# Optimization experiments

Measured on AMD Instinct MI355X. Metric: run time of the kernel, lower is better.

Reference implementation:

```python
import jax, jax.numpy as jnp
import numpy as np

EPS = 1e-5
EMBED_DIM = 1024
CTX_DIM = 768
NUM_HEADS = 16
DH = EMBED_DIM // NUM_HEADS
# Faithful to torch source: embed_dim // num_heads ** 0.5 parses as embed_dim // (num_heads**0.5)
SCALE = EMBED_DIM // (NUM_HEADS ** 0.5)  # = 256.0


def ws_conv1x1(x, w, b, mask):
    # weight-standardized 1x1 conv1d: w [O, I, 1], x [B, I, T]
    w2 = w[..., 0]
    mu = jnp.mean(w2, axis=1, keepdims=True)
    var = jnp.var(w2, axis=1, keepdims=True)
    wn = (w2 - mu) * jax.lax.rsqrt(var + EPS)
    y = jnp.einsum('oi,bit->bot', wn, x) + b[None, :, None]
    if mask is not None:
        y = jnp.where(mask, y, 0.0)  # mask [B,1,T] bool
    return y


def layernorm(x, g, b):
    # normalize over last axis
    mu = jnp.mean(x, axis=-1, keepdims=True)
    var = jnp.var(x, axis=-1, keepdims=True)
    return (x - mu) * jax.lax.rsqrt(var + EPS) * g + b


def setup_inputs() -> dict:
    key = jax.random.key(0)
    ks = jax.random.split(key, 16)
    B, T, S = 4, 1024, 1024
    inp = {
        'x': jax.random.normal(ks[0], (B, EMBED_DIM, T), dtype=jnp.float32),
        'context': jax.random.normal(ks[1], (B, CTX_DIM, S), dtype=jnp.float32),
        'mask': jax.random.randint(ks[2], (B, 1, T), 0, 2).astype(bool),
        'mask_ctx': jax.random.randint(ks[3], (B, 1, S), 0, 2).astype(bool),
        'qw': jax.random.normal(ks[4], (EMBED_DIM, EMBED_DIM, 1), dtype=jnp.float32) * 0.02,
        'qb': jnp.zeros((EMBED_DIM,), jnp.float32),
        'kw': jax.random.normal(ks[5], (EMBED_DIM, CTX_DIM, 1), dtype=jnp.float32) * 0.02,
        'kb': jnp.zeros((EMBED_DIM,), jnp.float32),
        'vw': jax.random.normal(ks[6], (EMBED_DIM, CTX_DIM, 1), dtype=jnp.float32) * 0.02,
        'vb': jnp.zeros((EMBED_DIM,), jnp.float32),
        'ow': jax.random.normal(ks[7], (EMBED_DIM, EMBED_DIM, 1), dtype=jnp.float32) * 0.02,
        'ob': jnp.zeros((EMBED_DIM,), jnp.float32),
        'gq': jnp.ones((DH,), jnp.float32), 'bq': jnp.zeros((DH,), jnp.float32),
        'gk': jnp.ones((DH,), jnp.float32), 'bk': jnp.zeros((DH,), jnp.float32),
        'gv': jnp.ones((DH,), jnp.float32), 'bv': jnp.zeros((DH,), jnp.float32),
    }
    return inp


def reference(x, context, mask, mask_ctx, qw, qb, kw, kb, vw, vb, ow, ob, gq, bq, gk, bk, gv, bv):
    B, E, T = x.shape
    S = context.shape[-1]
    q = ws_conv1x1(x, qw, qb, mask)            # [B,E,T]
    k = ws_conv1x1(context, kw, kb, mask_ctx)  # [B,E,S]
    v = ws_conv1x1(context, vw, vb, mask_ctx)  # [B,E,S]
    # split heads -> [B,H,dh,L]
    q = q.reshape(B, NUM_HEADS, DH, T)
    k = k.reshape(B, NUM_HEADS, DH, S)
    v = v.reshape(B, NUM_HEADS, DH, S)
    # middle_norm: LayerNorm over dh (applied on transposed layout)
    q = jnp.swapaxes(layernorm(jnp.swapaxes(q, -1, -2), gq, bq), -1, -2)
    k = jnp.swapaxes(layernorm(jnp.swapaxes(k, -1, -2), gk, bk), -1, -2)
    v = jnp.swapaxes(layernorm(jnp.swapaxes(v, -1, -2), gv, bv), -1, -2)
    # scores: k^T @ q -> [B,H,S,T]
    scores = jnp.einsum('bhds,bhdt->bhst', k, q) / SCALE
    scores = jnp.where(mask[:, :, None, :], scores, -1e9)  # mask over query dim T
    scores = jax.nn.softmax(scores, axis=-1)               # softmax over T (as in source)
    scores = jnp.where(mask_ctx[:, :, :, None], scores, 0.0)
    out = jnp.einsum('bhds,bhst->bhdt', v, scores)          # v @ scores -> [B,H,dh,T]
    out = out.reshape(B, E, T)
    out = ws_conv1x1(out, ow, ob, mask) + x
    return out
```

## Files before the change

kernel.cpp:

```cpp
#include <hip/hip_runtime.h>

#define NB 4
#define TT 1024
#define SS 1024
#define EE 1024
#define CCH 768
#define NH 16
#define DHH 64
#define EPSF 1e-5f
#define QSCALE (1.4426950408889634f / 256.0f)

typedef unsigned short u16;
typedef __attribute__((ext_vector_type(8))) short short8;
typedef __attribute__((ext_vector_type(8))) unsigned short u16x8;
typedef __attribute__((ext_vector_type(4))) unsigned short u16x4;
typedef __attribute__((ext_vector_type(4))) float f32x4;

__device__ __forceinline__ u16 f2bu(float f) {
    union { float f; unsigned u; } x; x.f = f;
    unsigned r = x.u + 0x7fffu + ((x.u >> 16) & 1u);
    return (u16)(r >> 16);
}
__device__ __forceinline__ float bu2f(u16 u) {
    union { unsigned u; float f; } x; x.u = ((unsigned)u) << 16; return x.f;
}

#if __has_builtin(__builtin_amdgcn_exp2f)
#define EXP2(x) __builtin_amdgcn_exp2f(x)
#else
#define EXP2(x) exp2f(x)
#endif

#define MFMA16(a, b, c) __builtin_amdgcn_mfma_f32_16x16x32_bf16((a), (b), (c), 0, 0, 0)

__device__ __forceinline__ void gload16(const void* g, void* l) {
    __builtin_amdgcn_global_load_lds(
        (const __attribute__((address_space(1))) void*)g,
        (__attribute__((address_space(3))) void*)l, 16, 0, 0);
}

template<int R>
__device__ __forceinline__ void stage_tile(
    const u16* __restrict__ g, int ldg, u16* lds, int w, int lane) {
    constexpr int PW = R / 32;
    int r0 = lane >> 3;
    int cs = ((lane & 7) << 4) ^ (r0 << 4);
#pragma unroll
    for (int j = 0; j < PW; j++) {
        int inst = w * PW + j;
        const u16* src = g + (size_t)(inst * 8 + r0) * ldg + (cs >> 1);
        gload16(src, lds + inst * 512);
    }
}

__device__ __forceinline__ const u16* swz_ptr(const u16* tile, int row, int col) {
    int off = row * 128 + ((col * 2) ^ ((row & 7) << 4));
    return (const u16*)((const char*)tile + off);
}

#define PREP_WS_END   4096
#define PREP_SCAN_END (PREP_WS_END + 8)
#define PREP_TR_END   (PREP_SCAN_END + 1792)
#define PREP_FILL_END (PREP_TR_END + 4096)

__global__ __launch_bounds__(256) void prep(
    const float* __restrict__ qw, const float* __restrict__ kw,
    const float* __restrict__ vw, const float* __restrict__ ow,
    u16* __restrict__ wqn, u16* __restrict__ wkn,
    u16* __restrict__ wvn, u16* __restrict__ won,
    const float* __restrict__ x, const float* __restrict__ ctx,
    const int* __restrict__ mask, const int* __restrict__ mask_ctx,
    u16* __restrict__ xc, u16* __restrict__ cc,
    int* __restrict__ tIdx, int* __restrict__ sIdx,
    int* __restrict__ cntQ, int* __restrict__ cntK,
    float* __restrict__ outF) {
    __shared__ float tile[64][65];
    __shared__ int spos[64], smask[64], wtoti[4];
    __shared__ float sa[4], sb2[4], smean, srstd;
    int bid = blockIdx.x, tid = threadIdx.x;

    if (bid < PREP_WS_END) {
        int mat = bid >> 10, row = bid & 1023;
        const float* w = mat == 0 ? qw : (mat == 1 ? kw : (mat == 2 ? vw : ow));
        u16* wn = mat == 0 ? wqn : (mat == 1 ? wkn : (mat == 2 ? wvn : won));
        int I = (mat == 1 || mat == 2) ? CCH : EE;
        const float* wr = w + (size_t)row * I;
        float s = 0.f, s2 = 0.f;
        for (int i = tid; i < I; i += 256) { float v = wr[i]; s += v; s2 += v * v; }
#pragma unroll
        for (int off = 32; off > 0; off >>= 1) { s += __shfl_down(s, off); s2 += __shfl_down(s2, off); }
        int wid = tid >> 6;
        if ((tid & 63) == 0) { sa[wid] = s; sb2[wid] = s2; }
        __syncthreads();
        if (tid == 0) {
            float ts = sa[0] + sa[1] + sa[2] + sa[3];
            float ts2 = sb2[0] + sb2[1] + sb2[2] + sb2[3];
            float mean = ts / (float)I;
            float var = ts2 / (float)I - mean * mean;
            smean = mean; srstd = rsqrtf(var + EPSF);
        }
        __syncthreads();
        float mean = smean, r = srstd;
        u16* wo = wn + (size_t)row * I;
        for (int i = tid; i < I; i += 256) wo[i] = f2bu((wr[i] - mean) * r);
        return;
    }
    if (bid < PREP_SCAN_END) {
        int t = bid - PREP_WS_END;
        int which = t & 1, b = t >> 1;
        const int* m = (which ? mask_ctx : mask) + b * 1024;
        int* idx = (which ? sIdx : tIdx) + b * 1024;
        int* cnt = (which ? cntK : cntQ) + b;
        int base = tid * 4;
        int v[4]; int s = 0;
#pragma unroll
        for (int i = 0; i < 4; i++) { v[i] = m[base + i] ? 1 : 0; s += v[i]; }
        int lane = tid & 63, wid = tid >> 6;
        int inc = s;
#pragma unroll
        for (int off = 1; off < 64; off <<= 1) {
            int o = __shfl_up(inc, off);
            if (lane >= off) inc += o;
        }
        if (lane == 63) wtoti[wid] = inc;
        __syncthreads();
        int woff = 0;
        for (int i = 0; i < wid; i++) woff += wtoti[i];
        int p = woff + inc - s;
#pragma unroll
        for (int i = 0; i < 4; i++) {
            if (v[i]) idx[p] = base + i;
            p += v[i];
        }
        if (tid == 255) *cnt = p;
        return;
    }
    if (bid < PREP_TR_END) {
        int t = bid - PREP_SCAN_END;
        int xb = t & 15; int rem = t >> 4;
        int yy = rem % 28, b = rem / 28;
        int mat = yy < 16 ? 0 : 1;
        int r0 = (mat == 0 ? yy : yy - 16) * 64;
        int R = mat == 0 ? EE : CCH;
        const float* in = mat == 0 ? x : ctx;
        const int* m = (mat == 0 ? mask : mask_ctx) + (size_t)b * 1024;
        u16* out = mat == 0 ? xc : cc;
        int c0 = xb * 64;
        const float* ip = in + (size_t)b * R * 1024;
        u16* op = out + (size_t)b * R * 1024;
#pragma unroll
        for (int mm = 0; mm < 16; mm++) {
            int id = tid + 256 * mm; int r = id >> 6, c = id & 63;
            tile[r][c] = ip[(size_t)(r0 + r) * 1024 + c0 + c];
        }
        int base = tid * 4;
        int v[4]; int s = 0;
#pragma unroll
        for (int i = 0; i < 4; i++) { v[i] = m[base + i] ? 1 : 0; s += v[i]; }
        int lane = tid & 63, wid = tid >> 6;
        int inc = s;
#pragma unroll
        for (int off = 1; off < 64; off <<= 1) {
            int o = __shfl_up(inc, off);
            if (lane >= off) inc += o;
        }
        if (lane == 63) wtoti[wid] = inc;
        __syncthreads();
        int woff = 0;
        for (int i = 0; i < wid; i++) woff += wtoti[i];
        int p = woff + inc - s;
#pragma unroll
        for (int i = 0; i < 4; i++) {
            int g = base + i;
            if (g >= c0 && g < c0 + 64) { spos[g - c0] = p; smask[g - c0] = v[i]; }
            p += v[i];
        }
        __syncthreads();
#pragma unroll
        for (int mm = 0; mm < 16; mm++) {
            int id = tid + 256 * mm; int rr = id >> 6, cc2 = id & 63;
            if (smask[rr])
                op[(size_t)spos[rr] * R + r0 + cc2] = f2bu(tile[cc2][rr]);
        }
        return;
    }
    {
        int f = bid - PREP_TR_END;
        int b = f >> 10, o = f & 1023;
        const float* xr = x + ((size_t)b * EE + o) * TT;
        float* orow = outF + ((size_t)b * EE + o) * TT;
        const int* mrow = mask + (size_t)b * TT;
        int4 mv = ((const int4*)mrow)[tid];
        float4 xv = ((const float4*)xr)[tid];
        int t4 = tid * 4;
        if (!mv.x) orow[t4 + 0] = xv.x;
        if (!mv.y) orow[t4 + 1] = xv.y;
        if (!mv.z) orow[t4 + 2] = xv.z;
        if (!mv.w) orow[t4 + 3] = xv.w;
    }
}

__device__ __forceinline__ void gemm_core(
    const u16* __restrict__ A, const u16* __restrict__ Bp, int I,
    int o0, int l0, u16 (*at)[128][64], u16 (*bt)[64][64], f32x4 (&acc)[4][2]) {
    int tid = threadIdx.x;
    int w = tid >> 6, lane = tid & 63, quad = lane >> 4, l16 = lane & 15;
    int wm = w & 1, wn = w >> 1;
    const u16* Ab = A + (size_t)o0 * I;
    const u16* Bb = Bp + (size_t)l0 * I;
    stage_tile<128>(Ab, I, &at[0][0][0], w, lane);
    stage_tile<64>(Bb, I, &bt[0][0][0], w, lane);
    __syncthreads();
    int cur = 0;
    for (int k0 = 0; k0 < I; k0 += 64, cur ^= 1) {
        int kn = k0 + 64;
        if (kn < I) {
            stage_tile<128>(Ab + kn, I, &at[cur ^ 1][0][0], w, lane);
            stage_tile<64>(Bb + kn, I, &bt[cur ^ 1][0][0], w, lane);
        }
#pragma unroll
        for (int ks = 0; ks < 64; ks += 32) {
            short8 af[4], bf[2];
#pragma unroll
            for (int i = 0; i < 4; i++)
                af[i] = *(const short8*)swz_ptr(&at[cur][0][0], wm * 64 + i * 16 + l16, ks + quad * 8);
#pragma unroll
            for (int j = 0; j < 2; j++)
                bf[j] = *(const short8*)swz_ptr(&bt[cur][0][0], wn * 32 + j * 16 + l16, ks + quad * 8);
#pragma unroll
            for (int mt = 0; mt < 4; mt++)
#pragma unroll
                for (int nt = 0; nt < 2; nt++)
                    acc[mt][nt] = MFMA16(af[mt], bf[nt], acc[mt][nt]);
        }
        __syncthreads();
    }
}

__global__ __launch_bounds__(256) void proj_qkv(
    const u16* __restrict__ wq, const u16* __restrict__ wk, const u16* __restrict__ wv,
    const u16* __restrict__ xc, const u16* __restrict__ cc,
    const float* __restrict__ qb, const float* __restrict__ kb, const float* __restrict__ vbi,
    const int* __restrict__ cntQ, const int* __restrict__ cntK,
    const float* __restrict__ gq, const float* __restrict__ bq,
    const float* __restrict__ gk, const float* __restrict__ bk,
    const float* __restrict__ gv, const float* __restrict__ bv,
    u16* __restrict__ qc, u16* __restrict__ kc, u16* __restrict__ vn) {
    int mat = blockIdx.x >> 3;
    int o0 = (blockIdx.x & 7) * 128;
    int l0 = blockIdx.y * 64;
    int b = blockIdx.z;
    int limit = (mat == 0) ? cntQ[b] : cntK[b];
    if (l0 >= limit) return;
    __shared__ u16 at[2][128][64];
    __shared__ u16 bt[2][64][64];
    __shared__ float sg[64], sbe[64], sbias[128];
    int tid = threadIdx.x;
    int w = tid >> 6, lane = tid & 63, quad = lane >> 4, l16 = lane & 15;
    int wm = w & 1, wn = w >> 1;
    const u16* A = mat == 0 ? wq : (mat == 1 ? wk : wv);
    const u16* BT = mat == 0 ? xc : cc;
    const float* bias = mat == 0 ? qb : (mat == 1 ? kb : vbi);
    int I = mat == 0 ? EE : CCH;
    if (tid < 64) {
        const float* gsrc = mat == 0 ? gq : (mat == 1 ? gk : gv);
        const float* bsrc = mat == 0 ? bq : (mat == 1 ? bk : bv);
        sg[tid] = gsrc[tid];
        sbe[tid] = bsrc[tid];
    }
    if (tid < 128) sbias[tid] = bias[o0 + tid];

    f32x4 acc[4][2] = {};
    gemm_core(A, BT + (size_t)b * 1024 * I, I, o0, l0, at, bt, acc);

    float scale = mat == 0 ? QSCALE : 1.0f;
    int h = (o0 >> 6) + wm;
    int bh = b * NH + h;
#pragma unroll
    for (int nt = 0; nt < 2; nt++) {
        int l = l0 + wn * 32 + nt * 16 + l16;
        float vbuf[16];
        float s = 0.f;
#pragma unroll
        for (int mt = 0; mt < 4; mt++)
#pragma unroll
            for (int reg = 0; reg < 4; reg++) {
                float v = acc[mt][nt][reg] + sbias[wm * 64 + mt * 16 + quad * 4 + reg];
                vbuf[mt * 4 + reg] = v; s += v;
            }
        s += __shfl_xor(s, 16); s += __shfl_xor(s, 32);
        float mean = s * (1.f / 64);
        float s2 = 0.f;
#pragma unroll
        for (int i = 0; i < 16; i++) { float dv = vbuf[i] - mean; s2 += dv * dv; }
        s2 += __shfl_xor(s2, 16); s2 += __shfl_xor(s2, 32);
        float r = rsqrtf(s2 * (1.f / 64) + EPSF);
        if (l < limit) {
            if (mat < 2) {
                u16* outT = mat == 0 ? qc : kc;
                u16* op = outT + ((size_t)bh * 1024 + l) * 64;
#pragma unroll
                for (int mt = 0; mt < 4; mt++) {
                    u16x4 pk;
#pragma unroll
                    for (int reg = 0; reg < 4; reg++) {
                        int d = mt * 16 + quad * 4 + reg;
                        pk[reg] = f2bu(((vbuf[mt * 4 + reg] - mean) * r * sg[d] + sbe[d]) * scale);
                    }
                    *(u16x4*)&op[mt * 16 + quad * 4] = pk;
                }
            } else {
#pragma unroll
                for (int mt = 0; mt < 4; mt++)
#pragma unroll
                    for (int reg = 0; reg < 4; reg++) {
                        int d = mt * 16 + quad * 4 + reg;
                        vn[((size_t)b * EE + h * 64 + d) * 1024 + l] =
                            f2bu((vbuf[mt * 4 + reg] - mean) * r * sg[d] + sbe[d]);
                    }
            }
        }
    }
}

__global__ __launch_bounds__(256) void attn_stats_mfma(
    const u16* __restrict__ qc, const u16* __restrict__ kc,
    const int* __restrict__ cntQ, const int* __restrict__ cntK,
    float* __restrict__ lneg) {
    int s0 = blockIdx.x * 64, h = blockIdx.y, b = blockIdx.z;
    int Sc = cntK[b], Tc = cntQ[b];
    if (s0 >= Sc) return;
    __shared__ u16 kt[64][64];
    __shared__ u16 qt[2][64][64];
    __shared__ float lp[4][64];
    int tid = threadIdx.x;
    int w = tid >> 6, lane = tid & 63, quad = lane >> 4, l16 = lane & 15;
    int head = b * NH + h;
    const u16* kp = kc + (size_t)head * SS * DHH;
    const u16* qp = qc + (size_t)head * TT * DHH;
    stage_tile<64>(kp + (size_t)s0 * DHH, DHH, &kt[0][0], w, lane);
    stage_tile<64>(qp, DHH, &qt[0][0][0], w, lane);
    __syncthreads();
    float rl[4][4] = {};
    int cur = 0;
    for (int t0 = 0; t0 < Tc; t0 += 64, cur ^= 1) {
        if (t0 + 64 < Tc)
            stage_tile<64>(qp + (size_t)(t0 + 64) * DHH, DHH, &qt[cur ^ 1][0][0], w, lane);
        f32x4 acc[4] = {};
#pragma unroll
        for (int ks = 0; ks < 64; ks += 32) {
            short8 bf = *(const short8*)swz_ptr(&qt[cur][0][0], w * 16 + l16, ks + quad * 8);
#pragma unroll
            for (int mt = 0; mt < 4; mt++) {
                short8 af = *(const short8*)swz_ptr(&kt[0][0], mt * 16 + l16, ks + quad * 8);
                acc[mt] = MFMA16(af, bf, acc[mt]);
            }
        }
        int tcol = t0 + w * 16 + l16;
        if (tcol < Tc) {
#pragma unroll
            for (int mt = 0; mt < 4; mt++)
#pragma unroll
                for (int reg = 0; reg < 4; reg++)
                    rl[mt][reg] += EXP2(acc[mt][reg]);
        }
        __syncthreads();
    }
#pragma unroll
    for (int mt = 0; mt < 4; mt++) {
#pragma unroll
        for (int reg = 0; reg < 4; reg++) {
            float v = rl[mt][reg];
            v += __shfl_xor(v, 1); v += __shfl_xor(v, 2);
            v += __shfl_xor(v, 4); v += __shfl_xor(v, 8);
            if (l16 == 0) lp[w][mt * 16 + quad * 4 + reg] = v;
        }
    }
    __syncthreads();
    if (tid < 64 && s0 + tid < Sc) {
        float lv = lp[0][tid] + lp[1][tid] + lp[2][tid] + lp[3][tid];
        lneg[(size_t)head * SS + s0 + tid] = -log2f(fmaxf(lv, 1e-30f));
    }
}

__global__ __launch_bounds__(256) void attn_pv_mfma(
    const u16* __restrict__ qc, const u16* __restrict__ kc, const u16* __restrict__ vn,
    const int* __restrict__ cntQ, const int* __restrict__ cntK,
    const float* __restrict__ lneg, u16* __restrict__ ac) {
    int t0 = blockIdx.x * 64, h = blockIdx.y, b = blockIdx.z;
    int Tc = cntQ[b], Sc = cntK[b];
    if (t0 >= Tc) return;
    __shared__ u16 qt[64][64];
    __shared__ u16 kt[2][64][64];
    __shared__ u16 vt[2][64][64];
    __shared__ u16 pt[64][72];
    __shared__ float sln[SS];
    int tid = threadIdx.x;
    int w = tid >> 6, lane = tid & 63, quad = lane >> 4, l16 = lane & 15;
    int head = b * NH + h;
    const u16* qp = qc + (size_t)head * TT * DHH;
    const u16* kp = kc + (size_t)head * SS * DHH;
    const u16* vp = vn + ((size_t)head * DHH) * SS;
    for (int i = tid; i < SS; i += 256) sln[i] = lneg[(size_t)head * SS + i];
    stage_tile<64>(qp + (size_t)t0 * DHH, DHH, &qt[0][0], w, lane);
    stage_tile<64>(kp, DHH, &kt[0][0][0], w, lane);
    stage_tile<64>(vp, SS, &vt[0][0][0], w, lane);
    __syncthreads();
    int tl = w * 16 + l16;
    f32x4 oacc[4] = {};
    int cur = 0;
    for (int s0 = 0; s0 < Sc; s0 += 64, cur ^= 1) {
        int sn = s0 + 64;
        if (sn < Sc) {
            stage_tile<64>(kp + (size_t)sn * DHH, DHH, &kt[cur ^ 1][0][0], w, lane);
            stage_tile<64>(vp + sn, SS, &vt[cur ^ 1][0][0], w, lane);
        }
        f32x4 acc[4] = {};
#pragma unroll
        for (int ks = 0; ks < 64; ks += 32) {
            short8 bf = *(const short8*)swz_ptr(&qt[0][0], tl, ks + quad * 8);
#pragma unroll
            for (int mt = 0; mt < 4; mt++) {
                short8 af = *(const short8*)swz_ptr(&kt[cur][0][0], mt * 16 + l16, ks + quad * 8);
                acc[mt] = MFMA16(af, bf, acc[mt]);
            }
        }
#pragma unroll
        for (int mt = 0; mt < 4; mt++) {
            u16x4 pk;
#pragma unroll
            for (int reg = 0; reg < 4; reg++) {
                int sl = mt * 16 + quad * 4 + reg;
                pk[reg] = (s0 + sl < Sc) ? f2bu(EXP2(acc[mt][reg] + sln[s0 + sl])) : (u16)0;
            }
            *(u16x4*)&pt[tl][mt * 16 + quad * 4] = pk;
        }
#pragma unroll
        for (int ks = 0; ks < 64; ks += 32) {
            short8 bf = *(const short8*)&pt[tl][ks + quad * 8];
#pragma unroll
            for (int mt = 0; mt < 4; mt++) {
                short8 af = *(const short8*)swz_ptr(&vt[cur][0][0], mt * 16 + l16, ks + quad * 8);
                oacc[mt] = MFMA16(af, bf, oacc[mt]);
            }
        }
        __syncthreads();
    }
#pragma unroll
    for (int mt = 0; mt < 4; mt++) {
        u16x4 pk;
#pragma unroll
        for (int reg = 0; reg < 4; reg++) pk[reg] = f2bu(oacc[mt][reg]);
        *(u16x4*)&pt[tl][mt * 16 + quad * 4] = pk;
    }
    __syncthreads();
#pragma unroll
    for (int i = 0; i < 2; i++) {
        int id = tid * 2 + i;
        int r = id >> 3, c = (id & 7) * 8;
        if (t0 + r < Tc)
            *(u16x8*)&ac[((size_t)b * TT + t0 + r) * EE + h * 64 + c] =
                *(const u16x8*)&pt[r][c];
    }
}

__global__ __launch_bounds__(256) void proj_o(
    const u16* __restrict__ won, const u16* __restrict__ ac,
    const float* __restrict__ obi, const int* __restrict__ tIdx,
    const int* __restrict__ cntQ, const float* __restrict__ x,
    float* __restrict__ out) {
    int o0 = blockIdx.x * 128, l0 = blockIdx.y * 64, b = blockIdx.z;
    int Tc = cntQ[b];
    if (l0 >= Tc) return;
    __shared__ u16 at[2][128][64];
    __shared__ u16 bt[2][64][64];
    __shared__ float sbias[128];
    __shared__ int stre[64];
    int tid = threadIdx.x;
    int w = tid >> 6, lane = tid & 63, quad = lane >> 4, l16 = lane & 15;
    int wm = w & 1, wn = w >> 1;
    if (tid < 128) sbias[tid] = obi[o0 + tid];
    if (tid < 64) stre[tid] = tIdx[(size_t)b * 1024 + l0 + tid];
    f32x4 acc[4][2] = {};
    gemm_core(won, ac + (size_t)b * TT * EE, EE, o0, l0, at, bt, acc);
#pragma unroll
    for (int nt = 0; nt < 2; nt++) {
        int lcol = wn * 32 + nt * 16 + l16;
        int l = l0 + lcol;
        if (l < Tc) {
            int treal = stre[lcol];
#pragma unroll
            for (int mt = 0; mt < 4; mt++)
#pragma unroll
                for (int reg = 0; reg < 4; reg++) {
                    int o = o0 + wm * 64 + mt * 16 + quad * 4 + reg;
                    size_t off = ((size_t)b * EE + o) * TT + treal;
                    out[off] = acc[mt][nt][reg] + sbias[wm * 64 + mt * 16 + quad * 4 + reg] + x[off];
                }
        }
    }
}

extern "C" void kernel_launch(void* const* d_in, const int* in_sizes, int n_in,
                              void* d_out, int out_size, void* d_ws, size_t ws_size,
                              hipStream_t stream) {
    const float* x        = (const float*)d_in[0];
    const float* ctx      = (const float*)d_in[1];
    const int*   mask     = (const int*)d_in[2];
    const int*   mask_ctx = (const int*)d_in[3];
    const float* qw  = (const float*)d_in[4];
    const float* qbi = (const float*)d_in[5];
    const float* kw  = (const float*)d_in[6];
    const float* kbi = (const float*)d_in[7];
    const float* vw  = (const float*)d_in[8];
    const float* vbi = (const float*)d_in[9];
    const float* ow  = (const float*)d_in[10];
    const float* obi = (const float*)d_in[11];
    const float* gq = (const float*)d_in[12];
    const float* bq = (const float*)d_in[13];
    const float* gk = (const float*)d_in[14];
    const float* bk = (const float*)d_in[15];
    const float* gv = (const float*)d_in[16];
    const float* bv = (const float*)d_in[17];

    u16* p = (u16*)d_ws;
    u16* wqn = p; p += (size_t)EE * EE;
    u16* wkn = p; p += (size_t)EE * CCH;
    u16* wvn = p; p += (size_t)EE * CCH;
    u16* won = p; p += (size_t)EE * EE;
    u16* xc  = p; p += (size_t)NB * TT * EE;
    u16* cc  = p; p += (size_t)NB * SS * CCH;
    u16* vn  = p; p += (size_t)NB * EE * SS;
    u16* qc  = p; p += (size_t)NB * NH * TT * DHH;
    u16* kc  = p; p += (size_t)NB * NH * SS * DHH;
    u16* ac  = p; p += (size_t)NB * TT * EE;
    float* lneg = (float*)p; p += (size_t)NB * NH * SS * 2;
    int* tIdx = (int*)p;
    int* sIdx = tIdx + NB * 1024;
    int* cntQ = sIdx + NB * 1024;
    int* cntK = cntQ + NB;

    prep<<<PREP_FILL_END, 256, 0, stream>>>(
        qw, kw, vw, ow, wqn, wkn, wvn, won, x, ctx, mask, mask_ctx,
        xc, cc, tIdx, sIdx, cntQ, cntK, (float*)d_out);

    proj_qkv<<<dim3(24, 16, NB), 256, 0, stream>>>(
        wqn, wkn, wvn, xc, cc, qbi, kbi, vbi, cntQ, cntK,
        gq, bq, gk, bk, gv, bv, qc, kc, vn);

    attn_stats_mfma<<<dim3(16, NH, NB), 256, 0, stream>>>(
        qc, kc, cntQ, cntK, lneg);

    attn_pv_mfma<<<dim3(16, NH, NB), 256, 0, stream>>>(
        qc, kc, vn, cntQ, cntK, lneg, ac);

    proj_o<<<dim3(8, 16, NB), 256, 0, stream>>>(
        won, ac, obi, tIdx, cntQ, x, (float*)d_out);
}
```

Before: 229.0 us.

## Materialize unnormalized probabilities and fold row-sum normalization into V

The stats kernel now writes the exp2 score matrix P to global memory as bf16 and rescales V columns by 1/rowsum in place. The PV kernel then becomes a plain V·P GEMM and no longer recomputes QK^T and exp. This trades roughly 128MB of P writes and reads for removing the duplicated score computation. Weight standardization also caches row values in registers instead of reading them twice.

```diff
diff --git a/kernel.cpp b/kernel.cpp
--- a/kernel.cpp
+++ b/kernel.cpp
@@ -85,8 +85,13 @@
         u16* wn = mat == 0 ? wqn : (mat == 1 ? wkn : (mat == 2 ? wvn : won));
         int I = (mat == 1 || mat == 2) ? CCH : EE;
         const float* wr = w + (size_t)row * I;
+        int nv = I >> 8;
+        float vals[4];
         float s = 0.f, s2 = 0.f;
-        for (int i = tid; i < I; i += 256) { float v = wr[i]; s += v; s2 += v * v; }
+        for (int j = 0; j < nv; j++) {
+            float v = wr[tid + 256 * j];
+            vals[j] = v; s += v; s2 += v * v;
+        }
 #pragma unroll
         for (int off = 32; off > 0; off >>= 1) { s += __shfl_down(s, off); s2 += __shfl_down(s2, off); }
         int wid = tid >> 6;
@@ -102,7 +107,7 @@
         __syncthreads();
         float mean = smean, r = srstd;
         u16* wo = wn + (size_t)row * I;
-        for (int i = tid; i < I; i += 256) wo[i] = f2bu((wr[i] - mean) * r);
+        for (int j = 0; j < nv; j++) wo[tid + 256 * j] = f2bu((vals[j] - mean) * r);
         return;
     }
     if (bid < PREP_SCAN_END) {
@@ -326,7 +331,7 @@
 __global__ __launch_bounds__(256) void attn_stats_mfma(
     const u16* __restrict__ qc, const u16* __restrict__ kc,
     const int* __restrict__ cntQ, const int* __restrict__ cntK,
-    float* __restrict__ lneg) {
+    u16* __restrict__ vn, u16* __restrict__ P) {
     int s0 = blockIdx.x * 64, h = blockIdx.y, b = blockIdx.z;
     int Sc = cntK[b], Tc = cntQ[b];
     if (s0 >= Sc) return;
@@ -338,6 +343,7 @@
     int head = b * NH + h;
     const u16* kp = kc + (size_t)head * SS * DHH;
     const u16* qp = qc + (size_t)head * TT * DHH;
+    u16* Pb = P + (size_t)head * TT * SS;
     stage_tile<64>(kp + (size_t)s0 * DHH, DHH, &kt[0][0], w, lane);
     stage_tile<64>(qp, DHH, &qt[0][0][0], w, lane);
     __syncthreads();
@@ -357,12 +363,18 @@
             }
         }
         int tcol = t0 + w * 16 + l16;
-        if (tcol < Tc) {
-#pragma unroll
-            for (int mt = 0; mt < 4; mt++)
-#pragma unroll
-                for (int reg = 0; reg < 4; reg++)
-                    rl[mt][reg] += EXP2(acc[mt][reg]);
+        int tok = tcol < Tc;
+#pragma unroll
+        for (int mt = 0; mt < 4; mt++) {
+            u16x4 pk;
+#pragma unroll
+            for (int reg = 0; reg < 4; reg++) {
+                int sl = s0 + mt * 16 + quad * 4 + reg;
+                float e = EXP2(acc[mt][reg]);
+                if (tok) rl[mt][reg] += e;
+                pk[reg] = (sl < Sc) ? f2bu(e) : (u16)0;
+            }
+            *(u16x4*)&Pb[(size_t)tcol * SS + s0 + mt * 16 + quad * 4] = pk;
         }
         __syncthreads();
     }
@@ -377,75 +389,63 @@
         }
     }
     __syncthreads();
-    if (tid < 64 && s0 + tid < Sc) {
-        float lv = lp[0][tid] + lp[1][tid] + lp[2][tid] + lp[3][tid];
-        lneg[(size_t)head * SS + s0 + tid] = -log2f(fmaxf(lv, 1e-30f));
+    {
+        int so = tid & 63, dg = tid >> 6;
+        int s = s0 + so;
+        float lv = lp[0][so] + lp[1][so] + lp[2][so] + lp[3][so];
+        float wsc = (lv > 0.f) ? (1.f / lv) : 0.f;
+        u16* vrow = vn + ((size_t)b * EE + h * 64) * SS;
+        int live = s < Sc;
+#pragma unroll
+        for (int i = 0; i < 16; i++) {
+            int d = dg * 16 + i;
+            size_t a = (size_t)d * SS + s;
+            vrow[a] = live ? f2bu(bu2f(vrow[a]) * wsc) : (u16)0;
+        }
     }
 }
 
 __global__ __launch_bounds__(256) void attn_pv_mfma(
-    const u16* __restrict__ qc, const u16* __restrict__ kc, const u16* __restrict__ vn,
+    const u16* __restrict__ vn, const u16* __restrict__ P,
     const int* __restrict__ cntQ, const int* __restrict__ cntK,
-    const float* __restrict__ lneg, u16* __restrict__ ac) {
+    u16* __restrict__ ac) {
     int t0 = blockIdx.x * 64, h = blockIdx.y, b = blockIdx.z;
     int Tc = cntQ[b], Sc = cntK[b];
     if (t0 >= Tc) return;
-    __shared__ u16 qt[64][64];
-    __shared__ u16 kt[2][64][64];
-    __shared__ u16 vt[2][64][64];
+    int Kc = (Sc + 63) & ~63;
+    __shared__ u16 at[2][64][64];
+    __shared__ u16 bt[2][64][64];
     __shared__ u16 pt[64][72];
-    __shared__ float sln[SS];
     int tid = threadIdx.x;
     int w = tid >> 6, lane = tid & 63, quad = lane >> 4, l16 = lane & 15;
     int head = b * NH + h;
-    const u16* qp = qc + (size_t)head * TT * DHH;
-    const u16* kp = kc + (size_t)head * SS * DHH;
     const u16* vp = vn + ((size_t)head * DHH) * SS;
-    for (int i = tid; i < SS; i += 256) sln[i] = lneg[(size_t)head * SS + i];
-    stage_tile<64>(qp + (size_t)t0 * DHH, DHH, &qt[0][0], w, lane);
-    stage_tile<64>(kp, DHH, &kt[0][0][0], w, lane);
-    stage_tile<64>(vp, SS, &vt[0][0][0], w, lane);
-    __syncthreads();
+    const u16* Pb = P + (size_t)head * TT * SS + (size_t)t0 * SS;
+    f32x4 oacc[4] = {};
+    if (Kc > 0) {
+        stage_tile<64>(vp, SS, &at[0][0][0], w, lane);
+        stage_tile<64>(Pb, SS, &bt[0][0][0], w, lane);
+        __syncthreads();
+        int cur = 0;
+        for (int k0 = 0; k0 < Kc; k0 += 64, cur ^= 1) {
+            int kn = k0 + 64;
+            if (kn < Kc) {
+                stage_tile<64>(vp + kn, SS, &at[cur ^ 1][0][0], w, lane);
+                stage_tile<64>(Pb + kn, SS, &bt[cur ^ 1][0][0], w, lane);
+            }
+#pragma unroll
+            for (int ks = 0; ks < 64; ks += 32) {
+                short8 bf = *(const short8*)swz_ptr(&bt[cur][0][0], w * 16 + l16, ks + quad * 8);
+#pragma unroll
+                for (int mt = 0; mt < 4; mt++) {
+                    short8 af = *(const short8*)swz_ptr(&at[cur][0][0], mt * 16 + l16, ks + quad * 8);
+                    oacc[mt] = MFMA16(af, bf, oacc[mt]);
+                }
+            }
+            __syncthreads();
+        }
+    }
     int tl = w * 16 + l16;
-    f32x4 oacc[4] = {};
-    int cur = 0;
-    for (int s0 = 0; s0 < Sc; s0 += 64, cur ^= 1) {
-        int sn = s0 + 64;
-        if (sn < Sc) {
-            stage_tile<64>(kp + (size_t)sn * DHH, DHH, &kt[cur ^ 1][0][0], w, lane);
-            stage_tile<64>(vp + sn, SS, &vt[cur ^ 1][0][0], w, lane);
-        }
-        f32x4 acc[4] = {};
-#pragma unroll
-        for (int ks = 0; ks < 64; ks += 32) {
-            short8 bf = *(const short8*)swz_ptr(&qt[0][0], tl, ks + quad * 8);
-#pragma unroll
-            for (int mt = 0; mt < 4; mt++) {
-                short8 af = *(const short8*)swz_ptr(&kt[cur][0][0], mt * 16 + l16, ks + quad * 8);
-                acc[mt] = MFMA16(af, bf, acc[mt]);
-            }
-        }
-#pragma unroll
-        for (int mt = 0; mt < 4; mt++) {
-            u16x4 pk;
-#pragma unroll
-            for (int reg = 0; reg < 4; reg++) {
-                int sl = mt * 16 + quad * 4 + reg;
-                pk[reg] = (s0 + sl < Sc) ? f2bu(EXP2(acc[mt][reg] + sln[s0 + sl])) : (u16)0;
-            }
-            *(u16x4*)&pt[tl][mt * 16 + quad * 4] = pk;
-        }
-#pragma unroll
-        for (int ks = 0; ks < 64; ks += 32) {
-            short8 bf = *(const short8*)&pt[tl][ks + quad * 8];
-#pragma unroll
-            for (int mt = 0; mt < 4; mt++) {
-                short8 af = *(const short8*)swz_ptr(&vt[cur][0][0], mt * 16 + l16, ks + quad * 8);
-                oacc[mt] = MFMA16(af, bf, oacc[mt]);
-            }
-        }
-        __syncthreads();
-    }
 #pragma unroll
     for (int mt = 0; mt < 4; mt++) {
         u16x4 pk;
@@ -534,7 +534,7 @@
     u16* qc  = p; p += (size_t)NB * NH * TT * DHH;
     u16* kc  = p; p += (size_t)NB * NH * SS * DHH;
     u16* ac  = p; p += (size_t)NB * TT * EE;
-    float* lneg = (float*)p; p += (size_t)NB * NH * SS * 2;
+    u16* P   = p; p += (size_t)NB * NH * TT * SS;
     int* tIdx = (int*)p;
     int* sIdx = tIdx + NB * 1024;
     int* cntQ = sIdx + NB * 1024;
@@ -549,10 +549,10 @@
         gq, bq, gk, bk, gv, bv, qc, kc, vn);
 
     attn_stats_mfma<<<dim3(16, NH, NB), 256, 0, stream>>>(
-        qc, kc, cntQ, cntK, lneg);
+        qc, kc, cntQ, cntK, vn, P);
 
     attn_pv_mfma<<<dim3(16, NH, NB), 256, 0, stream>>>(
-        qc, kc, vn, cntQ, cntK, lneg, ac);
+        vn, P, cntQ, cntK, ac);
 
     proj_o<<<dim3(8, 16, NB), 256, 0, stream>>>(
         won, ac, obi, tIdx, cntQ, x, (float*)d_out);
```

Result: no change. 227.1 us (-0.8%).
